# Kernel optimization log

Measured on AMD Instinct MI355X. Metric: run time of the kernel, lower is better.

## Reference

```python
import jax, jax.numpy as jnp
import numpy as np

STRIDE = 1
PADDING = 1


def setup_inputs() -> dict:
    key = jax.random.key(0)
    k1, k2, k3 = jax.random.split(key, 3)
    x = jax.random.normal(k1, (16, 64, 224, 224), dtype=jnp.float32)
    W = jax.random.normal(k2, (64, 64, 3, 3), dtype=jnp.float32)
    b = jax.random.normal(k3, (64,), dtype=jnp.float32)
    return {"x": x, "W": W, "b": b}


def reference(x, W, b):
    # Equivalent of the naive im2col+GEMM conv: a standard 2D convolution
    # (cross-correlation) with stride/padding, NCHW layout, OIHW weights.
    out = jax.lax.conv_general_dilated(
        x, W,
        window_strides=(STRIDE, STRIDE),
        padding=[(PADDING, PADDING), (PADDING, PADDING)],
        dimension_numbers=("NCHW", "OIHW", "NCHW"),
    )
    return out + b[None, :, None, None]
```

## Files before the change

kernel.cpp:

```cpp
#include <hip/hip_runtime.h>
#include <hip/hip_bf16.h>


typedef __attribute__((ext_vector_type(8)))  short   short8;
typedef __attribute__((ext_vector_type(8)))  unsigned short ushort8;
typedef __attribute__((ext_vector_type(16))) float   float16_t;

#define HW (224 * 224)

__device__ __forceinline__ unsigned short f2bf(float f) {
  __hip_bfloat16 h = __float2bfloat16(f);
  return *reinterpret_cast<unsigned short*>(&h);
}

__global__ void build_wt(const float* __restrict__ W, unsigned short* __restrict__ wt) {
  int i = blockIdx.x * 256 + threadIdx.x;
  if (i < 9 * 64 * 64) {
    int tap = i >> 12;
    int rem = i & 4095;
    int nn  = rem >> 6;
    int c   = rem & 63;
    wt[i] = f2bf(W[(nn * 64 + c) * 9 + tap]);
  }
}

__global__ __launch_bounds__(512, 4) void conv3x3_mfma(
    const float* __restrict__ x, const unsigned short* __restrict__ wt,
    const float* __restrict__ bias, float* __restrict__ out) {
  __shared__ __align__(16) unsigned short xs[18 * 8 * 34 * 8];

  const int bid = blockIdx.x;
  const int t   = (bid & 7) * 196 + (bid >> 3);
  const int bx  = t % 7;
  const int rem_t = t / 7;
  const int by  = rem_t % 14;
  const int img = rem_t / 14;

  const int w0  = bx * 32;
  const int h0  = by * 16;
  const int tid = threadIdx.x;
  const int lane = tid & 63, wave = tid >> 6;
  const int ln31 = lane & 31, lhi = lane >> 5;

  const float* xn = x + (size_t)img * 64 * HW;

  const int NITEMS = 18 * 8 * 34;
  for (int base = tid; base < NITEMS; base += 512 * 3) {
    float va[3][8];
    int   iw[3];
#pragma unroll
    for (int it = 0; it < 3; ++it) {
      const int i = base + it * 512;
      iw[it] = i;
      if (i < NITEMS) {
        const int h   = i / (8 * 34);
        const int rem = i - h * (8 * 34);
        const int cg  = rem / 34;
        const int w   = rem - cg * 34;
        const int gh  = h0 - 1 + h;
        const int gw  = w0 - 1 + w;
        if (((unsigned)gh < 224u) && ((unsigned)gw < 224u)) {
          const float* p = xn + (size_t)cg * 8 * HW + gh * 224 + gw;
#pragma unroll
          for (int j = 0; j < 8; ++j) va[it][j] = p[(size_t)j * HW];
        } else {
#pragma unroll
          for (int j = 0; j < 8; ++j) va[it][j] = 0.f;
        }
      }
    }
#pragma unroll
    for (int it = 0; it < 3; ++it) {
      if (iw[it] < NITEMS) {
        ushort8 pk;
#pragma unroll
        for (int j = 0; j < 8; ++j) pk[j] = f2bf(va[it][j]);
        *reinterpret_cast<ushort8*>(&xs[iw[it] * 8]) = pk;
      }
    }
  }
  __syncthreads();

  const int row0 = wave * 2;
  float16_t acc[2][2];
#pragma unroll
  for (int rb = 0; rb < 2; ++rb)
#pragma unroll
    for (int nb = 0; nb < 2; ++nb) acc[rb][nb] = 0.f;

#pragma unroll
  for (int r = 0; r < 3; ++r) {
#pragma unroll
    for (int s = 0; s < 3; ++s) {
      const int tap = r * 3 + s;
      short8 bq[4][2];
#pragma unroll
      for (int ks = 0; ks < 4; ++ks)
#pragma unroll
        for (int nb = 0; nb < 2; ++nb)
          bq[ks][nb] = *reinterpret_cast<const short8*>(
              wt + ((tap * 64 + nb * 32 + ln31) * 64 + ks * 16 + lhi * 8));

#pragma unroll
      for (int ks = 0; ks < 4; ++ks) {
        const int cg = ks * 2 + lhi;
#pragma unroll
        for (int rb = 0; rb < 2; ++rb) {
          const int hidx = row0 + rb + r;
          const int widx = ln31 + s;
          const short8 a = *reinterpret_cast<const short8*>(
              &xs[(((hidx * 8) + cg) * 34 + widx) * 8]);
          acc[rb][0] = __builtin_amdgcn_mfma_f32_32x32x16_bf16(a, bq[ks][0], acc[rb][0], 0, 0, 0);
          acc[rb][1] = __builtin_amdgcn_mfma_f32_32x32x16_bf16(a, bq[ks][1], acc[rb][1], 0, 0, 0);
        }
      }
    }
  }

#pragma unroll
  for (int rb = 0; rb < 2; ++rb) {
    const int h = h0 + row0 + rb;
#pragma unroll
    for (int nb = 0; nb < 2; ++nb) {
      const int ch = nb * 32 + ln31;
      const float bv = bias[ch];
      float* op = out + (((size_t)img * 64 + ch) * 224 + h) * 224 + w0;
#pragma unroll
      for (int q = 0; q < 4; ++q) {
        const int wloc = 8 * q + 4 * lhi;
        float4 v;
        v.x = acc[rb][nb][4 * q + 0] + bv;
        v.y = acc[rb][nb][4 * q + 1] + bv;
        v.z = acc[rb][nb][4 * q + 2] + bv;
        v.w = acc[rb][nb][4 * q + 3] + bv;
        *reinterpret_cast<float4*>(op + wloc) = v;
      }
    }
  }
}

#define TW 32
#define TH 32
#define KB 16
#define PXT 4
__global__ __launch_bounds__(256) void conv3x3_direct(
    const float* __restrict__ x, const float* __restrict__ wgt,
    const float* __restrict__ bias, float* __restrict__ out) {
  __shared__ float xsf[34 * 35];
  const int tx = blockIdx.x % 7, ty = blockIdx.x / 7;
  const int k0 = blockIdx.y * KB, n = blockIdx.z;
  const int w0 = tx * TW, h0 = ty * TH;
  const int tid = threadIdx.x;
  const int tw = tid & 7, th = tid >> 3;
  float acc[KB][PXT];
#pragma unroll
  for (int k = 0; k < KB; ++k)
#pragma unroll
    for (int p = 0; p < PXT; ++p) acc[k][p] = 0.f;
  const float* xn = x + (size_t)n * 64 * HW;
  for (int c = 0; c < 64; ++c) {
    const float* xc = xn + (size_t)c * HW;
    for (int i = tid; i < 34 * 34; i += 256) {
      int row = i / 34, col = i - row * 34;
      int gh = h0 - 1 + row, gw = w0 - 1 + col;
      float v = 0.f;
      if (gh >= 0 && gh < 224 && gw >= 0 && gw < 224) v = xc[gh * 224 + gw];
      xsf[row * 35 + col] = v;
    }
    __syncthreads();
    float in[3][6];
#pragma unroll
    for (int r = 0; r < 3; ++r)
#pragma unroll
      for (int q = 0; q < 6; ++q) in[r][q] = xsf[(th + r) * 35 + tw * PXT + q];
    const float* wc = wgt + ((size_t)k0 * 64 + c) * 9;
#pragma unroll
    for (int k = 0; k < KB; ++k) {
      const float* wk = wc + (size_t)k * 64 * 9;
#pragma unroll
      for (int r = 0; r < 3; ++r)
#pragma unroll
        for (int s = 0; s < 3; ++s) {
          float wv = wk[r * 3 + s];
#pragma unroll
          for (int p = 0; p < PXT; ++p) acc[k][p] += wv * in[r][s + p];
        }
    }
    __syncthreads();
  }
#pragma unroll
  for (int k = 0; k < KB; ++k) {
    float bv = bias[k0 + k];
    float4 v = make_float4(acc[k][0] + bv, acc[k][1] + bv, acc[k][2] + bv, acc[k][3] + bv);
    float* op = out + ((((size_t)n * 64 + (k0 + k)) * 224 + (h0 + th)) * 224 + (w0 + tw * PXT));
    *reinterpret_cast<float4*>(op) = v;
  }
}

extern "C" void kernel_launch(void* const* d_in, const int* in_sizes, int n_in,
                              void* d_out, int out_size, void* d_ws, size_t ws_size,
                              hipStream_t stream) {
  const float* x = (const float*)d_in[0];
  const float* W = (const float*)d_in[1];
  const float* b = (const float*)d_in[2];
  float* out = (float*)d_out;

  if (ws_size >= 9 * 64 * 64 * sizeof(unsigned short)) {
    unsigned short* wt = (unsigned short*)d_ws;
    build_wt<<<144, 256, 0, stream>>>(W, wt);
    conv3x3_mfma<<<1568, 512, 0, stream>>>(x, wt, b, out);
  } else {
    dim3 grid(7 * 7, 64 / KB, 16);
    conv3x3_direct<<<grid, 256, 0, stream>>>(x, W, b, out);
  }
}
```

Measured before the change: 487.1 us.

## Double-buffer input channel chunks in LDS to overlap loads with MFMA

Splits the 64 input channels into four 16-channel chunks and stages them in a two-slot LDS buffer. The next chunk's global loads are issued into registers before the current chunk's MFMAs run, then converted and written to the other slot afterwards. This hides global-load latency behind compute instead of loading the whole tile up front. The cost is extra registers for the prefetch (launch bounds lowered to 2 blocks/SM), one barrier per chunk, and clamped addresses for out-of-bounds loads.

```diff
diff --git a/kernel.cpp b/kernel.cpp
--- a/kernel.cpp
+++ b/kernel.cpp
@@ -24,10 +24,10 @@
   }
 }
 
-__global__ __launch_bounds__(512, 4) void conv3x3_mfma(
+__global__ __launch_bounds__(512, 2) void conv3x3_mfma(
     const float* __restrict__ x, const unsigned short* __restrict__ wt,
     const float* __restrict__ bias, float* __restrict__ out) {
-  __shared__ __align__(16) unsigned short xs[18 * 8 * 34 * 8];
+  __shared__ __align__(16) unsigned short xs[2][18 * 2 * 34 * 8];
 
   const int bid = blockIdx.x;
   const int t   = (bid & 7) * 196 + (bid >> 3);
@@ -44,77 +44,95 @@
 
   const float* xn = x + (size_t)img * 64 * HW;
 
-  const int NITEMS = 18 * 8 * 34;
-  for (int base = tid; base < NITEMS; base += 512 * 3) {
-    float va[3][8];
-    int   iw[3];
-#pragma unroll
-    for (int it = 0; it < 3; ++it) {
-      const int i = base + it * 512;
-      iw[it] = i;
-      if (i < NITEMS) {
-        const int h   = i / (8 * 34);
-        const int rem = i - h * (8 * 34);
-        const int cg  = rem / 34;
-        const int w   = rem - cg * 34;
+  for (int i = tid; i < 1224; i += 512) {
+    const int h   = i / 68;
+    const int rem = i - h * 68;
+    const int cgl = rem / 34;
+    const int w   = rem - cgl * 34;
+    const int gh  = h0 - 1 + h;
+    const int gw  = w0 - 1 + w;
+    ushort8 pk;
+    if (((unsigned)gh < 224u) && ((unsigned)gw < 224u)) {
+      const float* p = xn + (size_t)(cgl * 8) * HW + gh * 224 + gw;
+#pragma unroll
+      for (int j = 0; j < 8; ++j) pk[j] = f2bf(p[(size_t)j * HW]);
+    } else {
+#pragma unroll
+      for (int j = 0; j < 8; ++j) pk[j] = 0;
+    }
+    *reinterpret_cast<ushort8*>(&xs[0][i * 8]) = pk;
+  }
+  __syncthreads();
+
+  const int row0 = wave * 2;
+  float16_t acc[2][2];
+#pragma unroll
+  for (int rb = 0; rb < 2; ++rb)
+#pragma unroll
+    for (int nb = 0; nb < 2; ++nb) acc[rb][nb] = 0.f;
+
+#pragma unroll
+  for (int q = 0; q < 4; ++q) {
+    float pf[3][8];
+    bool  pin[3];
+    bool  pvw[3];
+    int   pidx[3];
+    if (q < 3) {
+#pragma unroll
+      for (int u = 0; u < 3; ++u) {
+        const int i  = tid + u * 512;
+        const bool vw = (i < 1224);
+        const int ii = vw ? i : 0;
+        const int h   = ii / 68;
+        const int rem = ii - h * 68;
+        const int cgl = rem / 34;
+        const int w   = rem - cgl * 34;
         const int gh  = h0 - 1 + h;
         const int gw  = w0 - 1 + w;
-        if (((unsigned)gh < 224u) && ((unsigned)gw < 224u)) {
-          const float* p = xn + (size_t)cg * 8 * HW + gh * 224 + gw;
-#pragma unroll
-          for (int j = 0; j < 8; ++j) va[it][j] = p[(size_t)j * HW];
-        } else {
-#pragma unroll
-          for (int j = 0; j < 8; ++j) va[it][j] = 0.f;
-        }
-      }
-    }
-#pragma unroll
-    for (int it = 0; it < 3; ++it) {
-      if (iw[it] < NITEMS) {
-        ushort8 pk;
-#pragma unroll
-        for (int j = 0; j < 8; ++j) pk[j] = f2bf(va[it][j]);
-        *reinterpret_cast<ushort8*>(&xs[iw[it] * 8]) = pk;
-      }
-    }
-  }
-  __syncthreads();
-
-  const int row0 = wave * 2;
-  float16_t acc[2][2];
-#pragma unroll
-  for (int rb = 0; rb < 2; ++rb)
-#pragma unroll
-    for (int nb = 0; nb < 2; ++nb) acc[rb][nb] = 0.f;
-
-#pragma unroll
-  for (int r = 0; r < 3; ++r) {
-#pragma unroll
-    for (int s = 0; s < 3; ++s) {
-      const int tap = r * 3 + s;
-      short8 bq[4][2];
-#pragma unroll
-      for (int ks = 0; ks < 4; ++ks)
-#pragma unroll
-        for (int nb = 0; nb < 2; ++nb)
-          bq[ks][nb] = *reinterpret_cast<const short8*>(
-              wt + ((tap * 64 + nb * 32 + ln31) * 64 + ks * 16 + lhi * 8));
-
-#pragma unroll
-      for (int ks = 0; ks < 4; ++ks) {
-        const int cg = ks * 2 + lhi;
+        const bool inb = vw && ((unsigned)gh < 224u) && ((unsigned)gw < 224u);
+        const int ghc = min(max(gh, 0), 223);
+        const int gwc = min(max(gw, 0), 223);
+        const float* p = xn + (size_t)(((q + 1) * 2 + cgl) * 8) * HW + ghc * 224 + gwc;
+#pragma unroll
+        for (int j = 0; j < 8; ++j) pf[u][j] = p[(size_t)j * HW];
+        pin[u] = inb; pvw[u] = vw; pidx[u] = ii;
+      }
+    }
+
+    const unsigned short* xq = &xs[q & 1][0];
+#pragma unroll
+    for (int r = 0; r < 3; ++r) {
+#pragma unroll
+      for (int s = 0; s < 3; ++s) {
+        const int tap = r * 3 + s;
+        const short8 b0 = *reinterpret_cast<const short8*>(
+            wt + ((tap * 64 + ln31) * 64 + q * 16 + lhi * 8));
+        const short8 b1 = *reinterpret_cast<const short8*>(
+            wt + ((tap * 64 + 32 + ln31) * 64 + q * 16 + lhi * 8));
 #pragma unroll
         for (int rb = 0; rb < 2; ++rb) {
           const int hidx = row0 + rb + r;
           const int widx = ln31 + s;
           const short8 a = *reinterpret_cast<const short8*>(
-              &xs[(((hidx * 8) + cg) * 34 + widx) * 8]);
-          acc[rb][0] = __builtin_amdgcn_mfma_f32_32x32x16_bf16(a, bq[ks][0], acc[rb][0], 0, 0, 0);
-          acc[rb][1] = __builtin_amdgcn_mfma_f32_32x32x16_bf16(a, bq[ks][1], acc[rb][1], 0, 0, 0);
+              &xq[((hidx * 2 + lhi) * 34 + widx) * 8]);
+          acc[rb][0] = __builtin_amdgcn_mfma_f32_32x32x16_bf16(a, b0, acc[rb][0], 0, 0, 0);
+          acc[rb][1] = __builtin_amdgcn_mfma_f32_32x32x16_bf16(a, b1, acc[rb][1], 0, 0, 0);
         }
       }
     }
+
+    if (q < 3) {
+#pragma unroll
+      for (int u = 0; u < 3; ++u) {
+        if (pvw[u]) {
+          ushort8 pk;
+#pragma unroll
+          for (int j = 0; j < 8; ++j) pk[j] = pin[u] ? f2bf(pf[u][j]) : (unsigned short)0;
+          *reinterpret_cast<ushort8*>(&xs[(q + 1) & 1][pidx[u] * 8]) = pk;
+        }
+      }
+    }
+    __syncthreads();
   }
 
 #pragma unroll
@@ -126,13 +144,13 @@
       const float bv = bias[ch];
       float* op = out + (((size_t)img * 64 + ch) * 224 + h) * 224 + w0;
 #pragma unroll
-      for (int q = 0; q < 4; ++q) {
-        const int wloc = 8 * q + 4 * lhi;
+      for (int qq = 0; qq < 4; ++qq) {
+        const int wloc = 8 * qq + 4 * lhi;
         float4 v;
-        v.x = acc[rb][nb][4 * q + 0] + bv;
-        v.y = acc[rb][nb][4 * q + 1] + bv;
-        v.z = acc[rb][nb][4 * q + 2] + bv;
-        v.w = acc[rb][nb][4 * q + 3] + bv;
+        v.x = acc[rb][nb][4 * qq + 0] + bv;
+        v.y = acc[rb][nb][4 * qq + 1] + bv;
+        v.z = acc[rb][nb][4 * qq + 2] + bv;
+        v.w = acc[rb][nb][4 * qq + 3] + bv;
         *reinterpret_cast<float4*>(op + wloc) = v;
       }
     }
```

After: 483.6 us. No clear change (-0.7%).
